# Kernel tuning notes

Hardware: AMD Instinct MI355X
Metric: run time of the kernel (lower is better)

The kernel has to match this reference:

```python
import jax, jax.numpy as jnp
import numpy as np

N_NODES = 100000
N_EDGES = 1600000
NUM_FEATURES = 128


def setup_inputs() -> dict:
    key = jax.random.key(0)
    ks = jax.random.split(key, 10)
    x = jax.random.normal(ks[0], (N_NODES, NUM_FEATURES), dtype=jnp.float32)
    edge_index = jax.random.randint(ks[1], (2, N_EDGES), 0, N_NODES, dtype=jnp.int64)
    # conv1 MLP: Linear(num_features,128) -> ReLU -> Linear(128,128)
    s1 = 1.0 / np.sqrt(NUM_FEATURES)
    W1 = jax.random.uniform(ks[2], (NUM_FEATURES, 128), jnp.float32, -s1, s1)
    b1 = jax.random.uniform(ks[3], (128,), jnp.float32, -s1, s1)
    s2 = 1.0 / np.sqrt(128)
    W2 = jax.random.uniform(ks[4], (128, 128), jnp.float32, -s2, s2)
    b2 = jax.random.uniform(ks[5], (128,), jnp.float32, -s2, s2)
    # conv2 MLP: Linear(128,64) -> ReLU -> Linear(64,64)
    W3 = jax.random.uniform(ks[6], (128, 64), jnp.float32, -s2, s2)
    b3 = jax.random.uniform(ks[7], (64,), jnp.float32, -s2, s2)
    s3 = 1.0 / np.sqrt(64)
    W4 = jax.random.uniform(ks[8], (64, 64), jnp.float32, -s3, s3)
    b4 = jax.random.uniform(ks[9], (64,), jnp.float32, -s3, s3)
    return {"x": x, "edge_index": edge_index, "W1": W1, "b1": b1,
            "W2": W2, "b2": b2, "W3": W3, "b3": b3, "W4": W4, "b4": b4}


def _gin_conv(x, src, dst, Wa, ba, Wb, bb):
    # GINConv with eps=0: out = MLP(x + sum_{j->i} x_j)
    agg = jax.ops.segment_sum(x[src], dst, num_segments=N_NODES)
    h = x + agg
    h = jax.nn.relu(h @ Wa + ba)
    return h @ Wb + bb


def reference(x, edge_index, W1, b1, W2, b2, W3, b3, W4, b4):
    src, dst = edge_index[0], edge_index[1]
    h = jax.nn.relu(_gin_conv(x, src, dst, W1, b1, W2, b2))
    h = jax.nn.relu(_gin_conv(h, src, dst, W3, b3, W4, b4))
    return h
```

## Files before the change

### kernel.cpp

```cpp
#include <hip/hip_runtime.h>
#include <hip/hip_bf16.h>

#define NODES 100000
#define EDGES 1600000
#define NBINS ((NODES + 127) >> 7)
#define BINCAP 2560
#define PB_BLOCKS 256
#define PB_CHUNK ((EDGES + PB_BLOCKS - 1) / PB_BLOCKS)
#define CAST_BLOCKS 12500
#define WPREP_BLOCKS 176

typedef __bf16 bf16x8 __attribute__((ext_vector_type(8)));
typedef float f32x4 __attribute__((ext_vector_type(4)));

__device__ __forceinline__ unsigned short f2b(float f) {
  __hip_bfloat16 h = __float2bfloat16(f);
  return __builtin_bit_cast(unsigned short, h);
}
__device__ __forceinline__ float b_lo(unsigned u) { return __uint_as_float(u << 16); }
__device__ __forceinline__ float b_hi(unsigned u) { return __uint_as_float(u & 0xffff0000u); }

__global__ __launch_bounds__(256) void prep_count(
    const float4* __restrict__ x4, ushort4* __restrict__ xh4,
    const float* __restrict__ W1, const float* __restrict__ W2,
    const float* __restrict__ W3, const float* __restrict__ W4,
    unsigned short* __restrict__ Wt1, unsigned short* __restrict__ Wt2,
    unsigned short* __restrict__ Wt3, unsigned short* __restrict__ Wt4,
    int* __restrict__ cnt) {
  const int b = blockIdx.x;
  if (b < CAST_BLOCKS) {
    int i = b * 256 + threadIdx.x;
    float4 v = x4[i];
    ushort4 o;
    o.x = f2b(v.x); o.y = f2b(v.y); o.z = f2b(v.z); o.w = f2b(v.w);
    xh4[i] = o;
    return;
  }
  if (b < CAST_BLOCKS + WPREP_BLOCKS) {
    int i = (b - CAST_BLOCKS) * 256 + threadIdx.x;
    if (i < 16384) {
      int n = i >> 7, k = i & 127;
      Wt1[i] = f2b(W1[k * 128 + n]);
    } else if (i < 32768) {
      int j = i - 16384; int n = j >> 7, k = j & 127;
      Wt2[j] = f2b(W2[k * 128 + n]);
    } else if (i < 40960) {
      int j = i - 32768; int n = j >> 7, k = j & 127;
      Wt3[j] = f2b(W3[k * 64 + n]);
    } else if (i < 45056) {
      int j = i - 40960; int n = j >> 6, k = j & 63;
      Wt4[j] = f2b(W4[k * 64 + n]);
    }
    return;
  }
  for (int i = threadIdx.x; i < NBINS; i += 256) cnt[i] = 0;
}

__global__ __launch_bounds__(256) void bin_scatter(const int* __restrict__ src,
                                                   const int* __restrict__ dst,
                                                   int* __restrict__ cnt,
                                                   unsigned* __restrict__ coarse) {
  __shared__ int base[NBINS];
  __shared__ int h[NBINS];
  const int beg = blockIdx.x * PB_CHUNK;
  const int end = min(beg + PB_CHUNK, EDGES);
  for (int i = threadIdx.x; i < NBINS; i += 256) h[i] = 0;
  __syncthreads();
  for (int e = beg + threadIdx.x; e < end; e += 256)
    atomicAdd(&h[dst[e] >> 7], 1);
  __syncthreads();
  for (int i = threadIdx.x; i < NBINS; i += 256) {
    int c = h[i];
    if (c > 0) base[i] = atomicAdd(&cnt[i], c);
    h[i] = 0;
  }
  __syncthreads();
  for (int e = beg + threadIdx.x; e < end; e += 256) {
    int d = dst[e];
    int b = d >> 7;
    int pos = base[b] + atomicAdd(&h[b], 1);
    coarse[(size_t)b * BINCAP + pos] = (unsigned)src[e] | ((unsigned)(d & 127) << 17);
  }
}

__global__ __launch_bounds__(256) void bin_fine(const unsigned* __restrict__ coarse,
                                                const int* __restrict__ cnt,
                                                int2* __restrict__ rowpairs,
                                                int* __restrict__ bucket) {
  __shared__ unsigned ent[BINCAP];
  __shared__ unsigned obuf[BINCAP];
  __shared__ int deg[128];
  __shared__ int pre[128];
  const int b = blockIdx.x;
  const int t = threadIdx.x;
  const int s0 = b * BINCAP;
  const int nE = cnt[b];
  const int binBase = b << 7;

  if (t < 128) deg[t] = 0;
  __syncthreads();
  for (int i = t; i < nE; i += 256) {
    unsigned e = coarse[s0 + i];
    ent[i] = e;
    atomicAdd(&deg[e >> 17], 1);
  }
  __syncthreads();
  int v = 0;
  if (t < 128) {
    v = deg[t];
    pre[t] = v;
  }
  __syncthreads();
  for (int off = 1; off < 128; off <<= 1) {
    int u = (t >= off && t < 128) ? pre[t - off] : 0;
    __syncthreads();
    if (t < 128) pre[t] += u;
    __syncthreads();
  }
  if (t < 128) {
    int inc = pre[t];
    int ex = inc - v;
    if (binBase + t < NODES) rowpairs[binBase + t] = make_int2(s0 + ex, s0 + inc);
    deg[t] = ex;
  }
  __syncthreads();
  for (int i = t; i < nE; i += 256) {
    unsigned e = ent[i];
    int pos = atomicAdd(&deg[e >> 17], 1);
    obuf[pos] = e & 0x1FFFFu;
  }
  __syncthreads();
  for (int i = t; i < nE; i += 256) bucket[s0 + i] = (int)obuf[i];
}

#define ACC8(r, m)                                                            \
  a[0] = fmaf(b_lo(r.x), m, a[0]); a[1] = fmaf(b_hi(r.x), m, a[1]);           \
  a[2] = fmaf(b_lo(r.y), m, a[2]); a[3] = fmaf(b_hi(r.y), m, a[3]);           \
  a[4] = fmaf(b_lo(r.z), m, a[4]); a[5] = fmaf(b_hi(r.z), m, a[5]);           \
  a[6] = fmaf(b_lo(r.w), m, a[6]); a[7] = fmaf(b_hi(r.w), m, a[7]);

template <int K, int N1, int N2, bool OUT_F32>
__global__ __launch_bounds__(256, 3) void gin_layer(
    const uint4* __restrict__ xq, const int2* __restrict__ rowpairs,
    const int* __restrict__ bucket,
    const unsigned short* __restrict__ Wa, const float* __restrict__ ba,
    const unsigned short* __restrict__ Wb, const float* __restrict__ bb,
    void* __restrict__ Cout, int M) {
  constexpr int LDA = K + 8;
  constexpr int LWA = K + 8;
  constexpr int LWB = N1 + 8;
  constexpr int NT1 = N1 / 16, KB1 = K / 32;
  constexpr int NT2 = N2 / 16, KB2 = N1 / 32;
  constexpr int WSH = (N1 * LWA > N2 * LWB) ? N1 * LWA : N2 * LWB;
  __shared__ unsigned short S[64 * LDA];
  __shared__ unsigned short Wl[WSH];

  const int tid = threadIdx.x;
  const int wave = tid >> 6;
  const int lane = tid & 63;
  const int g = lane >> 4;
  const int fl = lane & 15;
  const int rowBase = blockIdx.x * 64;

  for (int i = tid; i < N1 * (K / 8); i += 256) {
    int n = i / (K / 8), c = i % (K / 8);
    *(uint4*)&Wl[n * LWA + c * 8] = *(const uint4*)&Wa[(size_t)n * K + c * 8];
  }

  for (int p = 0; p < 4; p++) {
    const int rloc = wave * 16 + p * 4 + g;
    const int n = rowBase + rloc;
    float a[8] = {0.f, 0.f, 0.f, 0.f, 0.f, 0.f, 0.f, 0.f};
    if (n < M) {
      uint4 v = xq[(size_t)n * 16 + fl];
      a[0] = b_lo(v.x); a[1] = b_hi(v.x);
      a[2] = b_lo(v.y); a[3] = b_hi(v.y);
      a[4] = b_lo(v.z); a[5] = b_hi(v.z);
      a[6] = b_lo(v.w); a[7] = b_hi(v.w);
      const int2 se = rowpairs[n];
      const int beg = se.x, end = se.y;
      for (int j = beg; j < end; j += 8) {
        int i0 = j,     i1 = min(j + 1, end - 1), i2 = min(j + 2, end - 1),
            i3 = min(j + 3, end - 1), i4 = min(j + 4, end - 1),
            i5 = min(j + 5, end - 1), i6 = min(j + 6, end - 1),
            i7 = min(j + 7, end - 1);
        int s0 = bucket[i0], s1 = bucket[i1], s2 = bucket[i2], s3 = bucket[i3];
        int s4 = bucket[i4], s5 = bucket[i5], s6 = bucket[i6], s7 = bucket[i7];
        uint4 r0 = xq[(size_t)s0 * 16 + fl];
        uint4 r1 = xq[(size_t)s1 * 16 + fl];
        uint4 r2 = xq[(size_t)s2 * 16 + fl];
        uint4 r3 = xq[(size_t)s3 * 16 + fl];
        uint4 r4 = xq[(size_t)s4 * 16 + fl];
        uint4 r5 = xq[(size_t)s5 * 16 + fl];
        uint4 r6 = xq[(size_t)s6 * 16 + fl];
        uint4 r7 = xq[(size_t)s7 * 16 + fl];
        float m1 = (j + 1 < end) ? 1.f : 0.f;
        float m2 = (j + 2 < end) ? 1.f : 0.f;
        float m3 = (j + 3 < end) ? 1.f : 0.f;
        float m4 = (j + 4 < end) ? 1.f : 0.f;
        float m5 = (j + 5 < end) ? 1.f : 0.f;
        float m6 = (j + 6 < end) ? 1.f : 0.f;
        float m7 = (j + 7 < end) ? 1.f : 0.f;
        ACC8(r0, 1.f) ACC8(r1, m1) ACC8(r2, m2) ACC8(r3, m3)
        ACC8(r4, m4) ACC8(r5, m5) ACC8(r6, m6) ACC8(r7, m7)
      }
    }
    uint4 o;
    o.x = ((unsigned)f2b(a[1]) << 16) | f2b(a[0]);
    o.y = ((unsigned)f2b(a[3]) << 16) | f2b(a[2]);
    o.z = ((unsigned)f2b(a[5]) << 16) | f2b(a[4]);
    o.w = ((unsigned)f2b(a[7]) << 16) | f2b(a[6]);
    *(uint4*)&S[rloc * LDA + fl * 8] = o;
  }
  __syncthreads();

  const int arow = wave * 16 + fl;

  f32x4 acc[NT1];
#pragma unroll
  for (int c = 0; c < NT1; c++) acc[c] = (f32x4){0.f, 0.f, 0.f, 0.f};
#pragma unroll
  for (int kb = 0; kb < KB1; kb++) {
    bf16x8 av = *(const bf16x8*)&S[arow * LDA + kb * 32 + g * 8];
#pragma unroll
    for (int c = 0; c < NT1; c++) {
      bf16x8 bv = *(const bf16x8*)&Wl[(c * 16 + fl) * LWA + kb * 32 + g * 8];
      acc[c] = __builtin_amdgcn_mfma_f32_16x16x32_bf16(av, bv, acc[c], 0, 0, 0);
    }
  }

#pragma unroll
  for (int c = 0; c < NT1; c++) {
    int col = c * 16 + fl;
    float bv = ba[col];
#pragma unroll
    for (int reg = 0; reg < 4; reg++) {
      int rloc = wave * 16 + g * 4 + reg;
      S[rloc * LDA + col] = f2b(fmaxf(acc[c][reg] + bv, 0.f));
    }
  }
  __syncthreads();

  for (int i = tid; i < N2 * (N1 / 8); i += 256) {
    int n = i / (N1 / 8), c = i % (N1 / 8);
    *(uint4*)&Wl[n * LWB + c * 8] = *(const uint4*)&Wb[(size_t)n * N1 + c * 8];
  }
  __syncthreads();

  f32x4 acc2[NT2];
#pragma unroll
  for (int c = 0; c < NT2; c++) acc2[c] = (f32x4){0.f, 0.f, 0.f, 0.f};
#pragma unroll
  for (int kb = 0; kb < KB2; kb++) {
    bf16x8 av = *(const bf16x8*)&S[arow * LDA + kb * 32 + g * 8];
#pragma unroll
    for (int c = 0; c < NT2; c++) {
      bf16x8 bv = *(const bf16x8*)&Wl[(c * 16 + fl) * LWB + kb * 32 + g * 8];
      acc2[c] = __builtin_amdgcn_mfma_f32_16x16x32_bf16(av, bv, acc2[c], 0, 0, 0);
    }
  }

#pragma unroll
  for (int c = 0; c < NT2; c++) {
    int col = c * 16 + fl;
    float bv = bb[col];
#pragma unroll
    for (int reg = 0; reg < 4; reg++) {
      int row = rowBase + wave * 16 + g * 4 + reg;
      if (row < M) {
        float v = fmaxf(acc2[c][reg] + bv, 0.f);
        if (OUT_F32)
          ((float*)Cout)[(size_t)row * N2 + col] = v;
        else
          ((unsigned short*)Cout)[(size_t)row * N2 + col] = f2b(v);
      }
    }
  }
}

extern "C" void kernel_launch(void* const* d_in, const int* in_sizes, int n_in,
                              void* d_out, int out_size, void* d_ws, size_t ws_size,
                              hipStream_t stream) {
  const float* x = (const float*)d_in[0];
  const int* ei = (const int*)d_in[1];
  const int* src = ei;
  const int* dst = ei + EDGES;
  const float* W1 = (const float*)d_in[2];
  const float* b1 = (const float*)d_in[3];
  const float* W2 = (const float*)d_in[4];
  const float* b2 = (const float*)d_in[5];
  const float* W3 = (const float*)d_in[6];
  const float* b3 = (const float*)d_in[7];
  const float* W4 = (const float*)d_in[8];
  const float* b4 = (const float*)d_in[9];
  float* out = (float*)d_out;

  char* ws = (char*)d_ws;
  unsigned short* xh = (unsigned short*)ws;
  unsigned short* hB = xh + (size_t)NODES * 128;
  unsigned short* Wt1 = hB + (size_t)NODES * 128;
  unsigned short* Wt2 = Wt1 + 128 * 128;
  unsigned short* Wt3 = Wt2 + 128 * 128;
  unsigned short* Wt4 = Wt3 + 64 * 128;
  int2* rowpairs = (int2*)(Wt4 + 64 * 64);
  int* cnt = (int*)(rowpairs + NODES);
  unsigned* coarse = (unsigned*)(cnt + 784);
  int* bucket = (int*)(coarse + (size_t)NBINS * BINCAP);

  const int gblocks = (NODES + 63) / 64;

  prep_count<<<CAST_BLOCKS + WPREP_BLOCKS + 1, 256, 0, stream>>>(
      (const float4*)x, (ushort4*)xh, W1, W2, W3, W4, Wt1, Wt2, Wt3, Wt4, cnt);
  bin_scatter<<<PB_BLOCKS, 256, 0, stream>>>(src, dst, cnt, coarse);
  bin_fine<<<NBINS, 256, 0, stream>>>(coarse, cnt, rowpairs, bucket);

  gin_layer<128, 128, 128, false><<<gblocks, 256, 0, stream>>>(
      (const uint4*)xh, rowpairs, bucket, Wt1, b1, Wt2, b2, hB, NODES);
  gin_layer<128, 64, 64, true><<<gblocks, 256, 0, stream>>>(
      (const uint4*)hB, rowpairs, bucket, Wt3, b3, Wt4, b4, out, NODES);
}
```

Before: 315.2 us.

## Stage binned edges in LDS before coalesced writes; read GEMM weights from global

bin_scatter now runs 64 blocks that each process a larger edge chunk. Each block does a local prefix scan over the bins, sorts its payloads into a 100KB LDS buffer, then writes each bin's run to global memory contiguously, one wave per bin, instead of scattering single entries. gin_layer no longer copies weights into LDS. The MFMA B operands are loaded straight from global (L1/L2-cached), which drops the weight-staging loops and the block barriers, since each wave only touches its own rows of S. Launch bounds rise to 6 blocks per SM to use the freed LDS and registers. The risks are low parallelism in the scatter kernel and a higher cache/VMEM load from repeated weight fetches.

```diff
diff --git a/kernel.cpp b/kernel.cpp
--- a/kernel.cpp
+++ b/kernel.cpp
@@ -5,8 +5,8 @@
 #define EDGES 1600000
 #define NBINS ((NODES + 127) >> 7)
 #define BINCAP 2560
-#define PB_BLOCKS 256
-#define PB_CHUNK ((EDGES + PB_BLOCKS - 1) / PB_BLOCKS)
+#define SB_BLOCKS 64
+#define SB_CHUNK (EDGES / SB_BLOCKS)
 #define CAST_BLOCKS 12500
 #define WPREP_BLOCKS 176
 
@@ -60,26 +60,58 @@
                                                    const int* __restrict__ dst,
                                                    int* __restrict__ cnt,
                                                    unsigned* __restrict__ coarse) {
-  __shared__ int base[NBINS];
+  __shared__ unsigned pay[SB_CHUNK];
   __shared__ int h[NBINS];
-  const int beg = blockIdx.x * PB_CHUNK;
-  const int end = min(beg + PB_CHUNK, EDGES);
-  for (int i = threadIdx.x; i < NBINS; i += 256) h[i] = 0;
-  __syncthreads();
-  for (int e = beg + threadIdx.x; e < end; e += 256)
+  __shared__ int lofs[NBINS];
+  __shared__ int gbase[NBINS];
+  __shared__ int cur[NBINS];
+  __shared__ int ssc[256];
+  const int t = threadIdx.x;
+  const int beg = blockIdx.x * SB_CHUNK;
+  const int end = min(beg + SB_CHUNK, EDGES);
+
+  for (int i = t; i < NBINS; i += 256) h[i] = 0;
+  __syncthreads();
+  for (int e = beg + t; e < end; e += 256)
     atomicAdd(&h[dst[e] >> 7], 1);
   __syncthreads();
-  for (int i = threadIdx.x; i < NBINS; i += 256) {
+  int own = 0;
+  {
+    int lim = min(t * 4 + 4, NBINS);
+    for (int i = t * 4; i < lim; i++) own += h[i];
+    ssc[t] = own;
+  }
+  __syncthreads();
+  for (int off = 1; off < 256; off <<= 1) {
+    int u = (t >= off) ? ssc[t - off] : 0;
+    __syncthreads();
+    ssc[t] += u;
+    __syncthreads();
+  }
+  {
+    int run = ssc[t] - own;
+    int lim = min(t * 4 + 4, NBINS);
+    for (int i = t * 4; i < lim; i++) { lofs[i] = run; run += h[i]; }
+  }
+  for (int i = t; i < NBINS; i += 256) {
     int c = h[i];
-    if (c > 0) base[i] = atomicAdd(&cnt[i], c);
-    h[i] = 0;
-  }
-  __syncthreads();
-  for (int e = beg + threadIdx.x; e < end; e += 256) {
+    gbase[i] = (c > 0) ? atomicAdd(&cnt[i], c) : 0;
+    cur[i] = 0;
+  }
+  __syncthreads();
+  for (int e = beg + t; e < end; e += 256) {
     int d = dst[e];
     int b = d >> 7;
-    int pos = base[b] + atomicAdd(&h[b], 1);
-    coarse[(size_t)b * BINCAP + pos] = (unsigned)src[e] | ((unsigned)(d & 127) << 17);
+    int p = atomicAdd(&cur[b], 1);
+    pay[lofs[b] + p] = (unsigned)src[e] | ((unsigned)(d & 127) << 17);
+  }
+  __syncthreads();
+  const int wave = t >> 6, lane = t & 63;
+  for (int i = wave; i < NBINS; i += 4) {
+    int c = h[i];
+    int lo = lofs[i];
+    size_t gb = (size_t)i * BINCAP + gbase[i];
+    for (int l = lane; l < c; l += 64) coarse[gb + l] = pay[lo + l];
   }
 }
 
@@ -140,20 +172,16 @@
   a[6] = fmaf(b_lo(r.w), m, a[6]); a[7] = fmaf(b_hi(r.w), m, a[7]);
 
 template <int K, int N1, int N2, bool OUT_F32>
-__global__ __launch_bounds__(256, 3) void gin_layer(
+__global__ __launch_bounds__(256, 6) void gin_layer(
     const uint4* __restrict__ xq, const int2* __restrict__ rowpairs,
     const int* __restrict__ bucket,
     const unsigned short* __restrict__ Wa, const float* __restrict__ ba,
     const unsigned short* __restrict__ Wb, const float* __restrict__ bb,
     void* __restrict__ Cout, int M) {
   constexpr int LDA = K + 8;
-  constexpr int LWA = K + 8;
-  constexpr int LWB = N1 + 8;
   constexpr int NT1 = N1 / 16, KB1 = K / 32;
   constexpr int NT2 = N2 / 16, KB2 = N1 / 32;
-  constexpr int WSH = (N1 * LWA > N2 * LWB) ? N1 * LWA : N2 * LWB;
   __shared__ unsigned short S[64 * LDA];
-  __shared__ unsigned short Wl[WSH];
 
   const int tid = threadIdx.x;
   const int wave = tid >> 6;
@@ -161,11 +189,6 @@
   const int g = lane >> 4;
   const int fl = lane & 15;
   const int rowBase = blockIdx.x * 64;
-
-  for (int i = tid; i < N1 * (K / 8); i += 256) {
-    int n = i / (K / 8), c = i % (K / 8);
-    *(uint4*)&Wl[n * LWA + c * 8] = *(const uint4*)&Wa[(size_t)n * K + c * 8];
-  }
 
   for (int p = 0; p < 4; p++) {
     const int rloc = wave * 16 + p * 4 + g;
@@ -180,11 +203,11 @@
       const int2 se = rowpairs[n];
       const int beg = se.x, end = se.y;
       for (int j = beg; j < end; j += 8) {
-        int i0 = j,     i1 = min(j + 1, end - 1), i2 = min(j + 2, end - 1),
+        int i1 = min(j + 1, end - 1), i2 = min(j + 2, end - 1),
             i3 = min(j + 3, end - 1), i4 = min(j + 4, end - 1),
             i5 = min(j + 5, end - 1), i6 = min(j + 6, end - 1),
             i7 = min(j + 7, end - 1);
-        int s0 = bucket[i0], s1 = bucket[i1], s2 = bucket[i2], s3 = bucket[i3];
+        int s0 = bucket[j],  s1 = bucket[i1], s2 = bucket[i2], s3 = bucket[i3];
         int s4 = bucket[i4], s5 = bucket[i5], s6 = bucket[i6], s7 = bucket[i7];
         uint4 r0 = xq[(size_t)s0 * 16 + fl];
         uint4 r1 = xq[(size_t)s1 * 16 + fl];
@@ -212,7 +235,6 @@
     o.w = ((unsigned)f2b(a[7]) << 16) | f2b(a[6]);
     *(uint4*)&S[rloc * LDA + fl * 8] = o;
   }
-  __syncthreads();
 
   const int arow = wave * 16 + fl;
 
@@ -224,7 +246,7 @@
     bf16x8 av = *(const bf16x8*)&S[arow * LDA + kb * 32 + g * 8];
 #pragma unroll
     for (int c = 0; c < NT1; c++) {
-      bf16x8 bv = *(const bf16x8*)&Wl[(c * 16 + fl) * LWA + kb * 32 + g * 8];
+      bf16x8 bv = *(const bf16x8*)&Wa[(size_t)(c * 16 + fl) * K + kb * 32 + g * 8];
       acc[c] = __builtin_amdgcn_mfma_f32_16x16x32_bf16(av, bv, acc[c], 0, 0, 0);
     }
   }
@@ -239,13 +261,6 @@
       S[rloc * LDA + col] = f2b(fmaxf(acc[c][reg] + bv, 0.f));
     }
   }
-  __syncthreads();
-
-  for (int i = tid; i < N2 * (N1 / 8); i += 256) {
-    int n = i / (N1 / 8), c = i % (N1 / 8);
-    *(uint4*)&Wl[n * LWB + c * 8] = *(const uint4*)&Wb[(size_t)n * N1 + c * 8];
-  }
-  __syncthreads();
 
   f32x4 acc2[NT2];
 #pragma unroll
@@ -255,7 +270,7 @@
     bf16x8 av = *(const bf16x8*)&S[arow * LDA + kb * 32 + g * 8];
 #pragma unroll
     for (int c = 0; c < NT2; c++) {
-      bf16x8 bv = *(const bf16x8*)&Wl[(c * 16 + fl) * LWB + kb * 32 + g * 8];
+      bf16x8 bv = *(const bf16x8*)&Wb[(size_t)(c * 16 + fl) * N1 + kb * 32 + g * 8];
       acc2[c] = __builtin_amdgcn_mfma_f32_16x16x32_bf16(av, bv, acc2[c], 0, 0, 0);
     }
   }
@@ -311,7 +326,7 @@
 
   prep_count<<<CAST_BLOCKS + WPREP_BLOCKS + 1, 256, 0, stream>>>(
       (const float4*)x, (ushort4*)xh, W1, W2, W3, W4, Wt1, Wt2, Wt3, Wt4, cnt);
-  bin_scatter<<<PB_BLOCKS, 256, 0, stream>>>(src, dst, cnt, coarse);
+  bin_scatter<<<SB_BLOCKS, 256, 0, stream>>>(src, dst, cnt, coarse);
   bin_fine<<<NBINS, 256, 0, stream>>>(coarse, cnt, rowpairs, bucket);
 
   gin_layer<128, 128, 128, false><<<gblocks, 256, 0, stream>>>(
```

Result: slower. 481.3 us (+52.7%).
